# Kernel optimization log

Measured on AMD Instinct MI355X. Metric: run time of the kernel, lower is better.

## Reference

```python
import jax, jax.numpy as jnp
import numpy as np

COMMITMENT_COST = 0.25
TEMP = 0.1

def _normalize(x):
    # matches F.normalize(dim=-1): x / max(||x||, 1e-12)
    return x / jnp.maximum(jnp.linalg.norm(x, axis=-1, keepdims=True), 1e-12)

def setup_inputs() -> dict:
    key = jax.random.key(0)
    k1, k2 = jax.random.split(key)
    B, T, D, K = 16, 1024, 256, 4096
    inputs = jax.random.normal(k1, (B, T, D), dtype=jnp.float32)
    # embedding initialized N(0,1) then L2-normalized, as in __init__
    codebook = _normalize(jax.random.normal(k2, (K, D), dtype=jnp.float32))
    return {"inputs": inputs, "codebook": codebook}

def reference(inputs, codebook):
    K, D = codebook.shape
    flat = inputs.reshape(-1, D)                      # [N, D]
    flat_n = _normalize(flat)                         # [N, D]
    cb_n = jax.lax.stop_gradient(_normalize(codebook))  # [K, D] (weight.detach())
    # squared cosine distance: 2 - 2 * <x, e>
    dist = 2.0 - 2.0 * jnp.matmul(flat_n, cb_n.T)     # [N, K]
    soft_probs = jax.nn.softmax(-dist / TEMP, axis=1)  # [N, K]
    idx = jnp.argmin(dist, axis=1)                    # [N]
    # one-hot @ codebook == gather
    quantized = cb_n[idx].reshape(inputs.shape)       # [B, T, D]
    x_n = flat_n.reshape(inputs.shape)
    e_latent_loss = jnp.mean((jax.lax.stop_gradient(quantized) - x_n) ** 2)
    vq_loss = COMMITMENT_COST * e_latent_loss
    # straight-through estimator
    quant_st = x_n + jax.lax.stop_gradient(quantized - x_n)
    # perplexity from hard assignment histogram
    counts = jnp.zeros((K,), dtype=flat.dtype).at[idx].add(1.0)
    avg_probs = counts / flat.shape[0]
    perplexity = jnp.exp(-jnp.sum(avg_probs * jnp.log(avg_probs + 1e-10)))
    return vq_loss, quant_st, soft_probs, perplexity, idx[:, None]
```

## Files before the change

### kernel.cpp

```cpp
#include <hip/hip_runtime.h>
#include <cstdint>
#include <cstddef>

#define D_DIM 256
#define K_CODES 4096
#define N_ROWS 16384
#define NORM_ROWS_PER_BLK 32

typedef __attribute__((ext_vector_type(4))) int   i32x4;
typedef __attribute__((ext_vector_type(4))) float f32x4;

__device__ __forceinline__ unsigned short f2bf(float x) {
    const unsigned int u = __float_as_uint(x);
    return (unsigned short)((u + 0x7fffu + ((u >> 16) & 1u)) >> 16);
}
__device__ __forceinline__ float bf2f(unsigned short h) {
    return __uint_as_float((unsigned int)h << 16);
}

__device__ __forceinline__ void gload16(const unsigned short* g, unsigned short* l) {
    __builtin_amdgcn_global_load_lds(
        (const __attribute__((address_space(1))) void*)g,
        (__attribute__((address_space(3))) void*)l, 16, 0, 0);
}

#define MFMA(c, a, b) \
    asm volatile("v_mfma_f32_16x16x32_bf16 %0, %1, %2, %0" : "+v"(c) : "v"(a), "v"(b))

__device__ __forceinline__ float np_sumsq_128(const float* __restrict__ a)
{
    float r[8];
    #pragma unroll
    for (int j = 0; j < 8; ++j) r[j] = __fmul_rn(a[j], a[j]);
    #pragma unroll
    for (int i = 8; i < 128; i += 8)
        #pragma unroll
        for (int j = 0; j < 8; ++j)
            r[j] = __fadd_rn(r[j], __fmul_rn(a[i + j], a[i + j]));
    return __fadd_rn(__fadd_rn(__fadd_rn(r[0], r[1]), __fadd_rn(r[2], r[3])),
                     __fadd_rn(__fadd_rn(r[4], r[5]), __fadd_rn(r[6], r[7])));
}

__global__ __launch_bounds__(256) void norm_rows_np_kernel(
    const float* __restrict__ src, float* __restrict__ dst,
    unsigned short* __restrict__ dsth, unsigned short* __restrict__ dstl)
{
    __shared__ float lds[NORM_ROWS_PER_BLK * D_DIM];
    __shared__ float nrm[NORM_ROWS_PER_BLK];
    const int tid = threadIdx.x;
    const size_t base = (size_t)blockIdx.x * NORM_ROWS_PER_BLK * D_DIM;

    #pragma unroll
    for (int i = 0; i < NORM_ROWS_PER_BLK; ++i)
        lds[i * 256 + tid] = src[base + i * 256 + tid];
    __syncthreads();

    if (tid < NORM_ROWS_PER_BLK) {
        const float* row = &lds[tid * D_DIM];
        const float tot = __fadd_rn(np_sumsq_128(row), np_sumsq_128(row + 128));
        const float n = (float)sqrt((double)tot);
        nrm[tid] = fmaxf(n, 1e-12f);
    }
    __syncthreads();

    #pragma unroll
    for (int i = 0; i < NORM_ROWS_PER_BLK; ++i) {
        const int e = i * 256 + tid;
        const float v = lds[e] / nrm[i];
        dst[base + e] = v;
        const unsigned short h = f2bf(v);
        dsth[base + e] = h;
        dstl[base + e] = f2bf(v - bf2f(h));
    }
}

__global__ __launch_bounds__(256) void gemm_bf16x3_kernel(
    const unsigned short* __restrict__ Ah, const unsigned short* __restrict__ Al,
    const unsigned short* __restrict__ Bh, const unsigned short* __restrict__ Bl,
    float* __restrict__ C)
{
    __shared__ __align__(16) unsigned short smem[2 * 4 * 4096];

    const int tid  = threadIdx.x;
    const int lane = tid & 63;
    const int wv   = tid >> 6;
    const int wr   = wv >> 1, wc = wv & 1;

    const int GX  = K_CODES / 128;
    const int lin = blockIdx.y * GX + blockIdx.x;
    const int swz = (lin & 7) * (4096 / 8) + (lin >> 3);
    const int bm  = (swz / GX) * 128;
    const int bn  = (swz % GX) * 128;

    const int og0 = tid, og1 = 256 + tid;
    const int row0 = og0 >> 2, row1 = og1 >> 2;
    const int g0 = (og0 & 3) ^ ((row0 >> 1) & 3);
    const int g1 = (og1 & 3) ^ ((row1 >> 1) & 3);
    const size_t asrc0 = (size_t)(bm + row0) * D_DIM + g0 * 8;
    const size_t asrc1 = (size_t)(bm + row1) * D_DIM + g1 * 8;
    const size_t bsrc0 = (size_t)(bn + row0) * D_DIM + g0 * 8;
    const size_t bsrc1 = (size_t)(bn + row1) * D_DIM + g1 * 8;

    int aoff[4], boff[4];
    #pragma unroll
    for (int i = 0; i < 4; ++i) {
        const int ar = wr * 64 + i * 16 + (lane & 15);
        aoff[i] = ar * 64 + ((((lane >> 4) ^ ((ar >> 1) & 3)) & 3) << 4);
        const int br = wc * 64 + i * 16 + (lane & 15);
        boff[i] = br * 64 + ((((lane >> 4) ^ ((br >> 1) & 3)) & 3) << 4);
    }
    const char* sA = (const char*)smem;

    auto stage = [&](int buf, int k0) {
        unsigned short* l0 = smem + buf * 16384 + wv * 512;
        unsigned short* l1 = smem + buf * 16384 + 2048 + wv * 512;
        gload16(Ah + asrc0 + k0, l0);
        gload16(Ah + asrc1 + k0, l1);
        gload16(Al + asrc0 + k0, l0 + 4096);
        gload16(Al + asrc1 + k0, l1 + 4096);
        gload16(Bh + bsrc0 + k0, l0 + 8192);
        gload16(Bh + bsrc1 + k0, l1 + 8192);
        gload16(Bl + bsrc0 + k0, l0 + 12288);
        gload16(Bl + bsrc1 + k0, l1 + 12288);
    };

    f32x4 acc[4][4] = {};

    stage(0, 0);
    stage(1, 32);

    #pragma unroll
    for (int t = 0; t < 8; ++t) {
        const int b = t & 1;
        if (t < 7) asm volatile("s_waitcnt vmcnt(8)" ::: "memory");
        else       asm volatile("s_waitcnt vmcnt(0)" ::: "memory");
        __builtin_amdgcn_s_barrier();
        __builtin_amdgcn_sched_barrier(0);

        const char* base = sA + b * 32768;
        i32x4 ah[4], al[4], bh[4], bl[4];
        #pragma unroll
        for (int i = 0; i < 4; ++i) {
            ah[i] = *(const i32x4*)(base +         aoff[i]);
            al[i] = *(const i32x4*)(base +  8192 + aoff[i]);
            bh[i] = *(const i32x4*)(base + 16384 + boff[i]);
            bl[i] = *(const i32x4*)(base + 24576 + boff[i]);
        }
        asm volatile("s_waitcnt lgkmcnt(0)" ::: "memory");
        __builtin_amdgcn_sched_barrier(0);
        __builtin_amdgcn_s_barrier();
        __builtin_amdgcn_sched_barrier(0);

        if (t < 6) stage(b, (t + 2) * 32);

        __builtin_amdgcn_s_setprio(1);
        #pragma unroll
        for (int i = 0; i < 4; ++i)
            #pragma unroll
            for (int j = 0; j < 4; ++j)
                MFMA(acc[i][j], ah[i], bh[j]);
        #pragma unroll
        for (int i = 0; i < 4; ++i)
            #pragma unroll
            for (int j = 0; j < 4; ++j)
                MFMA(acc[i][j], ah[i], bl[j]);
        #pragma unroll
        for (int i = 0; i < 4; ++i)
            #pragma unroll
            for (int j = 0; j < 4; ++j)
                MFMA(acc[i][j], al[i], bh[j]);
        __builtin_amdgcn_s_setprio(0);
    }
    asm volatile("s_nop 7\n\ts_nop 7\n\ts_nop 7");

    #pragma unroll
    for (int i = 0; i < 4; ++i) {
        const int r0 = bm + wr * 64 + i * 16 + ((lane >> 4) << 2);
        #pragma unroll
        for (int j = 0; j < 4; ++j) {
            const int c0 = bn + wc * 64 + j * 16 + (lane & 15);
            #pragma unroll
            for (int r = 0; r < 4; ++r)
                C[(size_t)(r0 + r) * K_CODES + c0] = acc[i][j][r];
        }
    }
}

__global__ __launch_bounds__(256) void rowpass_kernel(
    float* __restrict__ P,
    const float* __restrict__ cbn,
    float* __restrict__ xq,
    float* __restrict__ idx_out,
    float* __restrict__ counts,
    float* __restrict__ rowloss)
{
    const int row = blockIdx.x;
    const int t = threadIdx.x;
    float4* rp = (float4*)(P + (size_t)row * K_CODES);

    __shared__ float sf[4];
    __shared__ float sbd[4];
    __shared__ float s_x[D_DIM];
    __shared__ int   s_cnt;
    __shared__ int   s_cand[128];
    __shared__ float s_dex[128];
    __shared__ int   s_besti;

    float vals[16];
    #pragma unroll
    for (int j = 0; j < 4; ++j) {
        const float4 v = rp[j * 256 + t];
        vals[j * 4 + 0] = v.x; vals[j * 4 + 1] = v.y;
        vals[j * 4 + 2] = v.z; vals[j * 4 + 3] = v.w;
    }

    s_x[t] = xq[(size_t)row * D_DIM + t];
    if (t == 0) s_cnt = 0;

    float m = -1e30f, bd = 3.402823466e+38f;
    #pragma unroll
    for (int i = 0; i < 16; ++i) {
        m = fmaxf(m, vals[i]);
        bd = fminf(bd, 2.0f - 2.0f * vals[i]);
    }
    #pragma unroll
    for (int off = 32; off > 0; off >>= 1) {
        m  = fmaxf(m,  __shfl_down(m,  off));
        bd = fminf(bd, __shfl_down(bd, off));
    }
    if ((t & 63) == 0) { sf[t >> 6] = m; sbd[t >> 6] = bd; }
    __syncthreads();
    const float M  = fmaxf(fmaxf(sf[0], sf[1]), fmaxf(sf[2], sf[3]));
    const float fb = fminf(fminf(sbd[0], sbd[1]), fminf(sbd[2], sbd[3]));

    const float TAU = 0.0078125f;
    #pragma unroll
    for (int i = 0; i < 16; ++i) {
        const float d = 2.0f - 2.0f * vals[i];
        if (d <= fb + TAU) {
            const int p = atomicAdd(&s_cnt, 1);
            if (p < 128) s_cand[p] = ((i >> 2) * 256 + t) * 4 + (i & 3);
        }
    }
    __syncthreads();
    const int cnt = min(s_cnt, 128);
    if (cnt == 1) {
        if (t == 0) s_besti = s_cand[0];
    } else {
        if (t < cnt) {
            const float* cb = cbn + (size_t)s_cand[t] * D_DIM;
            float acc = 0.0f;
            for (int k = 0; k < D_DIM; ++k) acc = fmaf(s_x[k], cb[k], acc);
            s_dex[t] = 2.0f - 2.0f * acc;
        }
        __syncthreads();
        if (t == 0) {
            float bdx = 3.402823466e+38f; int bii = 0x7fffffff;
            for (int c = 0; c < cnt; ++c) {
                const float d = s_dex[c]; const int ii = s_cand[c];
                if (d < bdx || (d == bdx && ii < bii)) { bdx = d; bii = ii; }
            }
            s_besti = bii;
        }
    }
    __syncthreads();
    const int besti = s_besti;

    float esum = 0.0f;
    #pragma unroll
    for (int i = 0; i < 16; ++i) {
        vals[i] = __expf(20.0f * (vals[i] - M));
        esum += vals[i];
    }
    #pragma unroll
    for (int off = 32; off > 0; off >>= 1) esum += __shfl_down(esum, off);
    __syncthreads();
    if ((t & 63) == 0) sf[t >> 6] = esum;
    __syncthreads();
    const float inv = 1.0f / (sf[0] + sf[1] + sf[2] + sf[3]);
    #pragma unroll
    for (int j = 0; j < 4; ++j) {
        rp[j * 256 + t] = make_float4(vals[j * 4 + 0] * inv, vals[j * 4 + 1] * inv,
                                      vals[j * 4 + 2] * inv, vals[j * 4 + 3] * inv);
    }

    const float q = cbn[(size_t)besti * D_DIM + t];
    xq[(size_t)row * D_DIM + t] = q;
    const float dd = q - s_x[t];
    float ls = dd * dd;
    #pragma unroll
    for (int off = 32; off > 0; off >>= 1) ls += __shfl_down(ls, off);
    __syncthreads();
    if ((t & 63) == 0) sf[t >> 6] = ls;
    __syncthreads();
    if (t == 0) {
        rowloss[row] = sf[0] + sf[1] + sf[2] + sf[3];
        idx_out[row] = (float)besti;
        atomicAdd(&counts[besti], 1.0f);
    }
}

__global__ __launch_bounds__(256) void finalize_kernel(
    const float* __restrict__ rowloss, const float* __restrict__ counts,
    float* __restrict__ out_loss, float* __restrict__ out_ppl)
{
    const int t = threadIdx.x;
    float s = 0.0f;
    for (int i = t; i < N_ROWS; i += 256) s += rowloss[i];
    float e = 0.0f;
    for (int i = t; i < K_CODES; i += 256) {
        const float avg = counts[i] * (1.0f / (float)N_ROWS);
        e += avg * logf(avg + 1e-10f);
    }
    #pragma unroll
    for (int off = 32; off > 0; off >>= 1) {
        s += __shfl_down(s, off);
        e += __shfl_down(e, off);
    }
    __shared__ float sf[4], se[4];
    if ((t & 63) == 0) { sf[t >> 6] = s; se[t >> 6] = e; }
    __syncthreads();
    if (t == 0) {
        out_loss[0] = 0.25f * (sf[0] + sf[1] + sf[2] + sf[3]) /
                      ((float)N_ROWS * (float)D_DIM);
        out_ppl[0] = expf(-(se[0] + se[1] + se[2] + se[3]));
    }
}

extern "C" void kernel_launch(void* const* d_in, const int* in_sizes, int n_in,
                              void* d_out, int out_size, void* d_ws, size_t ws_size,
                              hipStream_t stream) {
    const float* inputs   = (const float*)d_in[0];
    const float* codebook = (const float*)d_in[1];
    float* out = (float*)d_out;

    float* vq_loss = out;
    float* quant   = out + 1;
    float* probs   = quant + (size_t)N_ROWS * D_DIM;
    float* ppl     = probs + (size_t)N_ROWS * K_CODES;
    float* idxout  = ppl + 1;

    float* cbn     = (float*)d_ws;
    float* counts  = cbn + (size_t)K_CODES * D_DIM;
    float* rowloss = counts + K_CODES;
    unsigned short* Ah = (unsigned short*)(rowloss + N_ROWS);
    unsigned short* Al = Ah + (size_t)N_ROWS * D_DIM;
    unsigned short* Bh = Al + (size_t)N_ROWS * D_DIM;
    unsigned short* Bl = Bh + (size_t)K_CODES * D_DIM;

    hipMemsetAsync(counts, 0, K_CODES * sizeof(float), stream);
    norm_rows_np_kernel<<<K_CODES / NORM_ROWS_PER_BLK, 256, 0, stream>>>(codebook, cbn, Bh, Bl);
    norm_rows_np_kernel<<<N_ROWS / NORM_ROWS_PER_BLK, 256, 0, stream>>>(inputs, quant, Ah, Al);
    gemm_bf16x3_kernel<<<dim3(K_CODES / 128, N_ROWS / 128), 256, 0, stream>>>(Ah, Al, Bh, Bl, probs);
    rowpass_kernel<<<N_ROWS, 256, 0, stream>>>(probs, cbn, quant, idxout, counts, rowloss);
    finalize_kernel<<<1, 256, 0, stream>>>(rowloss, counts, vq_loss, ppl);
}
```

Measured before the change: 550.3 us.

## Process one row per wavefront in rowpass and restructure GEMM barrier placement

```diff
diff --git a/kernel.cpp b/kernel.cpp
--- a/kernel.cpp
+++ b/kernel.cpp
@@ -146,14 +146,6 @@
             bh[i] = *(const i32x4*)(base + 16384 + boff[i]);
             bl[i] = *(const i32x4*)(base + 24576 + boff[i]);
         }
-        asm volatile("s_waitcnt lgkmcnt(0)" ::: "memory");
-        __builtin_amdgcn_sched_barrier(0);
-        __builtin_amdgcn_s_barrier();
-        __builtin_amdgcn_sched_barrier(0);
-
-        if (t < 6) stage(b, (t + 2) * 32);
-
-        __builtin_amdgcn_s_setprio(1);
         #pragma unroll
         for (int i = 0; i < 4; ++i)
             #pragma unroll
@@ -169,7 +161,12 @@
             #pragma unroll
             for (int j = 0; j < 4; ++j)
                 MFMA(acc[i][j], al[i], bh[j]);
-        __builtin_amdgcn_s_setprio(0);
+
+        __builtin_amdgcn_sched_barrier(0);
+        __builtin_amdgcn_s_barrier();
+        __builtin_amdgcn_sched_barrier(0);
+
+        if (t < 6) stage(b, (t + 2) * 32);
     }
     asm volatile("s_nop 7\n\ts_nop 7\n\ts_nop 7");
 
@@ -194,33 +191,30 @@
     float* __restrict__ counts,
     float* __restrict__ rowloss)
 {
-    const int row = blockIdx.x;
-    const int t = threadIdx.x;
+    const int w = threadIdx.x >> 6;
+    const int l = threadIdx.x & 63;
+    const int row = blockIdx.x * 4 + w;
     float4* rp = (float4*)(P + (size_t)row * K_CODES);
 
-    __shared__ float sf[4];
-    __shared__ float sbd[4];
-    __shared__ float s_x[D_DIM];
-    __shared__ int   s_cnt;
-    __shared__ int   s_cand[128];
-    __shared__ float s_dex[128];
-    __shared__ int   s_besti;
-
-    float vals[16];
-    #pragma unroll
-    for (int j = 0; j < 4; ++j) {
-        const float4 v = rp[j * 256 + t];
+    __shared__ float s_x[4][D_DIM];
+    __shared__ int   s_cand[4][128];
+    __shared__ int   s_cnt[4];
+
+    float vals[64];
+    #pragma unroll
+    for (int j = 0; j < 16; ++j) {
+        const float4 v = rp[j * 64 + l];
         vals[j * 4 + 0] = v.x; vals[j * 4 + 1] = v.y;
         vals[j * 4 + 2] = v.z; vals[j * 4 + 3] = v.w;
     }
-
-    s_x[t] = xq[(size_t)row * D_DIM + t];
-    if (t == 0) s_cnt = 0;
+    const float4 xv4 = *(const float4*)&xq[(size_t)row * D_DIM + l * 4];
+    *(float4*)&s_x[w][l * 4] = xv4;
+    if (l == 0) s_cnt[w] = 0;
 
     float m = -1e30f, bd = 3.402823466e+38f;
     #pragma unroll
-    for (int i = 0; i < 16; ++i) {
-        m = fmaxf(m, vals[i]);
+    for (int i = 0; i < 64; ++i) {
+        m  = fmaxf(m, vals[i]);
         bd = fminf(bd, 2.0f - 2.0f * vals[i]);
     }
     #pragma unroll
@@ -228,73 +222,66 @@
         m  = fmaxf(m,  __shfl_down(m,  off));
         bd = fminf(bd, __shfl_down(bd, off));
     }
-    if ((t & 63) == 0) { sf[t >> 6] = m; sbd[t >> 6] = bd; }
-    __syncthreads();
-    const float M  = fmaxf(fmaxf(sf[0], sf[1]), fmaxf(sf[2], sf[3]));
-    const float fb = fminf(fminf(sbd[0], sbd[1]), fminf(sbd[2], sbd[3]));
+    const float M  = __shfl(m, 0);
+    const float fb = __shfl(bd, 0);
 
     const float TAU = 0.0078125f;
     #pragma unroll
-    for (int i = 0; i < 16; ++i) {
+    for (int i = 0; i < 64; ++i) {
         const float d = 2.0f - 2.0f * vals[i];
         if (d <= fb + TAU) {
-            const int p = atomicAdd(&s_cnt, 1);
-            if (p < 128) s_cand[p] = ((i >> 2) * 256 + t) * 4 + (i & 3);
-        }
-    }
-    __syncthreads();
-    const int cnt = min(s_cnt, 128);
+            const int p = atomicAdd(&s_cnt[w], 1);
+            if (p < 128) s_cand[w][p] = ((i >> 2) * 64 + l) * 4 + (i & 3);
+        }
+    }
+    const int cnt = min(s_cnt[w], 128);
+
+    int besti;
     if (cnt == 1) {
-        if (t == 0) s_besti = s_cand[0];
+        besti = s_cand[w][0];
     } else {
-        if (t < cnt) {
-            const float* cb = cbn + (size_t)s_cand[t] * D_DIM;
-            float acc = 0.0f;
-            for (int k = 0; k < D_DIM; ++k) acc = fmaf(s_x[k], cb[k], acc);
-            s_dex[t] = 2.0f - 2.0f * acc;
-        }
-        __syncthreads();
-        if (t == 0) {
-            float bdx = 3.402823466e+38f; int bii = 0x7fffffff;
-            for (int c = 0; c < cnt; ++c) {
-                const float d = s_dex[c]; const int ii = s_cand[c];
-                if (d < bdx || (d == bdx && ii < bii)) { bdx = d; bii = ii; }
-            }
-            s_besti = bii;
-        }
-    }
-    __syncthreads();
-    const int besti = s_besti;
+        float bdx = 3.402823466e+38f; int bii = 0x7fffffff;
+        for (int c = l; c < cnt; c += 64) {
+            const int ii = s_cand[w][c];
+            const float* cb = cbn + (size_t)ii * D_DIM;
+            float a = 0.0f;
+            for (int k = 0; k < D_DIM; ++k) a = fmaf(s_x[w][k], cb[k], a);
+            const float d = 2.0f - 2.0f * a;
+            if (d < bdx || (d == bdx && ii < bii)) { bdx = d; bii = ii; }
+        }
+        #pragma unroll
+        for (int off = 32; off > 0; off >>= 1) {
+            const float od = __shfl_down(bdx, off);
+            const int   oi = __shfl_down(bii, off);
+            if (od < bdx || (od == bdx && oi < bii)) { bdx = od; bii = oi; }
+        }
+        besti = __shfl(bii, 0);
+    }
 
     float esum = 0.0f;
     #pragma unroll
-    for (int i = 0; i < 16; ++i) {
+    for (int i = 0; i < 64; ++i) {
         vals[i] = __expf(20.0f * (vals[i] - M));
         esum += vals[i];
     }
     #pragma unroll
     for (int off = 32; off > 0; off >>= 1) esum += __shfl_down(esum, off);
-    __syncthreads();
-    if ((t & 63) == 0) sf[t >> 6] = esum;
-    __syncthreads();
-    const float inv = 1.0f / (sf[0] + sf[1] + sf[2] + sf[3]);
-    #pragma unroll
-    for (int j = 0; j < 4; ++j) {
-        rp[j * 256 + t] = make_float4(vals[j * 4 + 0] * inv, vals[j * 4 + 1] * inv,
-                                      vals[j * 4 + 2] * inv, vals[j * 4 + 3] * inv);
-    }
-
-    const float q = cbn[(size_t)besti * D_DIM + t];
-    xq[(size_t)row * D_DIM + t] = q;
-    const float dd = q - s_x[t];
-    float ls = dd * dd;
+    const float inv = 1.0f / __shfl(esum, 0);
+    #pragma unroll
+    for (int j = 0; j < 16; ++j) {
+        rp[j * 64 + l] = make_float4(vals[j * 4 + 0] * inv, vals[j * 4 + 1] * inv,
+                                     vals[j * 4 + 2] * inv, vals[j * 4 + 3] * inv);
+    }
+
+    const float4 q4 = *(const float4*)&cbn[(size_t)besti * D_DIM + l * 4];
+    *(float4*)&xq[(size_t)row * D_DIM + l * 4] = q4;
+    const float d0 = q4.x - xv4.x, d1 = q4.y - xv4.y;
+    const float d2 = q4.z - xv4.z, d3 = q4.w - xv4.w;
+    float ls = d0 * d0 + d1 * d1 + d2 * d2 + d3 * d3;
     #pragma unroll
     for (int off = 32; off > 0; off >>= 1) ls += __shfl_down(ls, off);
-    __syncthreads();
-    if ((t & 63) == 0) sf[t >> 6] = ls;
-    __syncthreads();
-    if (t == 0) {
-        rowloss[row] = sf[0] + sf[1] + sf[2] + sf[3];
+    if (l == 0) {
+        rowloss[row] = ls;
         idx_out[row] = (float)besti;
         atomicAdd(&counts[besti], 1.0f);
     }
@@ -352,6 +339,6 @@
     norm_rows_np_kernel<<<K_CODES / NORM_ROWS_PER_BLK, 256, 0, stream>>>(codebook, cbn, Bh, Bl);
     norm_rows_np_kernel<<<N_ROWS / NORM_ROWS_PER_BLK, 256, 0, stream>>>(inputs, quant, Ah, Al);
     gemm_bf16x3_kernel<<<dim3(K_CODES / 128, N_ROWS / 128), 256, 0, stream>>>(Ah, Al, Bh, Bl, probs);
-    rowpass_kernel<<<N_ROWS, 256, 0, stream>>>(probs, cbn, quant, idxout, counts, rowloss);
+    rowpass_kernel<<<N_ROWS / 4, 256, 0, stream>>>(probs, cbn, quant, idxout, counts, rowloss);
     finalize_kernel<<<1, 256, 0, stream>>>(rowloss, counts, vq_loss, ppl);
 }
```

Result: no change. 549.0 us (-0.2%).
